# Performance work log

Hardware: AMD Instinct MI355X
Metric: run time of the kernel (lower is better)

## Reference

```python
import jax, jax.numpy as jnp
import numpy as np

N = 100000      # num_nodes
R = 8           # num_relations
D = 128         # hidden_dim
E = 600000      # num_edges
P = 100000      # num query pairs
PH = 128        # pair_hidden_dim


def _xavier(key, shape):
    fan_in, fan_out = shape[-2], shape[-1]
    limit = float(np.sqrt(6.0 / (fan_in + fan_out)))
    return jax.random.uniform(key, shape, jnp.float32, -limit, limit)


def setup_inputs() -> dict:
    key = jax.random.key(0)
    ks = jax.random.split(key, 16)
    edge_index = jax.random.randint(ks[0], (2, E), 0, N)
    edge_type = jax.random.randint(ks[1], (E,), 0, R)
    drug_index = jax.random.randint(ks[2], (P,), 0, N)
    disease_index = jax.random.randint(ks[3], (P,), 0, N)
    emb = _xavier(ks[4], (N, D))
    rw1 = _xavier(ks[5], (R, D, D))
    sl1 = _xavier(ks[6], (D, D))
    b1 = jnp.zeros((D,), jnp.float32)
    rw2 = _xavier(ks[7], (R, D, D))
    sl2 = _xavier(ks[8], (D, D))
    b2 = jnp.zeros((D,), jnp.float32)
    pw1 = _xavier(ks[9], (3 * D, PH))
    pb1 = jnp.zeros((PH,), jnp.float32)
    pw2 = _xavier(ks[10], (PH, 1))
    pb2 = jnp.zeros((1,), jnp.float32)
    return {
        "edge_index": edge_index, "edge_type": edge_type,
        "drug_index": drug_index, "disease_index": disease_index,
        "emb": emb, "rw1": rw1, "sl1": sl1, "b1": b1,
        "rw2": rw2, "sl2": sl2, "b2": b2,
        "pw1": pw1, "pb1": pb1, "pw2": pw2, "pb2": pb2,
    }


def _rgcn_layer(x, rel_w, self_w, bias, src, dst, etype):
    # Transform all node features once per relation: [R, N, D]
    xW = jnp.einsum('nd,rde->rne', x, rel_w)
    # Per-relation in-degree of dst (matches torch bincount-per-relation, clamp_min(1))
    seg_key = etype * N + dst                                  # [E]
    deg = jax.ops.segment_sum(jnp.ones((src.shape[0],), x.dtype), seg_key,
                              num_segments=R * N)
    deg = jnp.maximum(deg, 1.0)
    msg = xW[etype, src] / deg[seg_key][:, None]               # [E, D]
    agg = jax.ops.segment_sum(msg, dst, num_segments=N)        # [N, D]
    return x @ self_w + agg + bias


def reference(edge_index, edge_type, drug_index, disease_index,
              emb, rw1, sl1, b1, rw2, sl2, b2, pw1, pb1, pw2, pb2):
    src, dst = edge_index[0], edge_index[1]
    # encode (eval mode: dropout is identity)
    x = _rgcn_layer(emb, rw1, sl1, b1, src, dst, edge_type)
    x = jax.nn.relu(x)
    x = _rgcn_layer(x, rw2, sl2, b2, src, dst, edge_type)
    # score_pairs
    dh = x[drug_index]
    sh = x[disease_index]
    feat = jnp.concatenate((dh, sh, dh * sh), axis=-1)         # [P, 3D]
    h = jax.nn.relu(feat @ pw1 + pb1)
    logits = (h @ pw2 + pb2)[:, 0]                             # [P]
    return logits
```

## Files before the change

kernel.cpp:

```cpp
#include <hip/hip_runtime.h>

#define D 128
#define RMAX 16

typedef short s16x8 __attribute__((ext_vector_type(8)));
typedef float f32x4 __attribute__((ext_vector_type(4)));

__device__ inline unsigned short f2b(float f) {
    unsigned u = __builtin_bit_cast(unsigned, f);
    unsigned r = (u + 0x7FFFu + ((u >> 16) & 1u)) >> 16;
    return (unsigned short)r;
}
__device__ inline float b2f(unsigned short h) {
    unsigned u = ((unsigned)h) << 16;
    return __builtin_bit_cast(float, u);
}


__global__ void k_count2(const int* __restrict__ etype, const int* __restrict__ dstA,
                         int E, int N, int R,
                         int* __restrict__ deg, int* __restrict__ counts) {
    __shared__ int lh[RMAX];
    if (threadIdx.x < RMAX) lh[threadIdx.x] = 0;
    __syncthreads();
    int e = blockIdx.x * blockDim.x + threadIdx.x;
    if (e < E) {
        int r = etype[e];
        atomicAdd(&deg[r * N + dstA[e]], 1);
        atomicAdd(&lh[r], 1);
    }
    __syncthreads();
    if (threadIdx.x < R && lh[threadIdx.x])
        atomicAdd(&counts[threadIdx.x], lh[threadIdx.x]);
}

__global__ void k_offsets(const int* __restrict__ counts, int* __restrict__ po,
                          int R, int N) {
    if (threadIdx.x == 0 && blockIdx.x == 0) {
        int acc = 0;
        for (int r = 0; r < R; ++r) {
            po[r] = acc;
            acc += ((counts[r] + 127) / 128) * 128;
        }
        po[R] = acc;
        acc += ((N + 127) / 128) * 128;
        po[R + 1] = acc;
    }
}


template<int VPT>
__global__ void k_scan_blk(const int* __restrict__ in, int* __restrict__ tmp,
                           int* __restrict__ bsum, int n) {
    __shared__ int sd[256];
    int t = threadIdx.x;
    long base = (long)blockIdx.x * (256 * VPT) + (long)t * VPT;
    int s[VPT];
    int tsum = 0;
    #pragma unroll
    for (int k = 0; k < VPT; ++k) { s[k] = (base + k < n) ? in[base + k] : 0; tsum += s[k]; }
    sd[t] = tsum;
    __syncthreads();
    for (int off = 1; off < 256; off <<= 1) {
        int v = (t >= off) ? sd[t - off] : 0;
        __syncthreads();
        sd[t] += v;
        __syncthreads();
    }
    int run = sd[t] - tsum;
    #pragma unroll
    for (int k = 0; k < VPT; ++k) { if (base + k < n) tmp[base + k] = run; run += s[k]; }
    if (t == 255) bsum[blockIdx.x] = sd[255];
}

__global__ void k_scan2(const int* __restrict__ bsum, int* __restrict__ boff, int nb) {
    __shared__ int sd[256];
    int t = threadIdx.x;
    int v = (t < nb) ? bsum[t] : 0;
    sd[t] = v;
    __syncthreads();
    for (int off = 1; off < 256; off <<= 1) {
        int w = (t >= off) ? sd[t - off] : 0;
        __syncthreads();
        sd[t] += w;
        __syncthreads();
    }
    if (t < nb) boff[t] = sd[t] - v;
}

__global__ void k_scan3(const int* __restrict__ tmp, const int* __restrict__ boff,
                        int* __restrict__ out, int n, int shift) {
    int i = blockIdx.x * 256 + threadIdx.x;
    if (i < n) out[i] = tmp[i] + boff[i >> shift];
}


__global__ void k_scatter3(const int* __restrict__ etype, const int* __restrict__ srcA,
                           const int* __restrict__ dstA, int E, int N, int R,
                           const int* __restrict__ degOff, const int* __restrict__ po,
                           int* __restrict__ binCur, int* __restrict__ slotSrc) {
    int t = blockIdx.x * 256 + threadIdx.x;
    if (t < E) {
        int r = etype[t];
        int bin = r * N + dstA[t];
        int rank = atomicAdd(&binCur[bin], 1);
        int pos = po[r] + (degOff[bin] - degOff[r * N]) + rank;
        slotSrc[pos] = srcA[t];
    } else if (t < E + N) {
        int n = t - E;
        slotSrc[po[R] + n] = n;
    }
}


__global__ void k_prep(const float* __restrict__ emb,
                       const float* __restrict__ rw1, const float* __restrict__ sl1,
                       const float* __restrict__ rw2, const float* __restrict__ sl2,
                       const float* __restrict__ pw1,
                       unsigned short* __restrict__ embb,
                       unsigned short* __restrict__ wAll1,
                       unsigned short* __restrict__ wAll2,
                       unsigned short* __restrict__ pw1T,
                       int N, int R)
{
    long t = (long)blockIdx.x * 256 + threadIdx.x;
    long u0 = (long)N * D / 4;
    if (t < u0) {
        long i = t * 4;
        f32x4 v = *(const f32x4*)(emb + i);
        unsigned a0 = (unsigned)f2b(v[0]) | ((unsigned)f2b(v[1]) << 16);
        unsigned a1 = (unsigned)f2b(v[2]) | ((unsigned)f2b(v[3]) << 16);
        uint2 o; o.x = a0; o.y = a1;
        *(uint2*)(embb + i) = o;
        return;
    }
    t -= u0;
    long uW = (long)(R + 1) * D * D;
    if (t < 2 * uW) {
        const float* rw = (t < uW) ? rw1 : rw2;
        const float* sl = (t < uW) ? sl1 : sl2;
        unsigned short* o = (t < uW) ? wAll1 : wAll2;
        long u = (t < uW) ? t : t - uW;
        int r = (int)(u >> 14);
        int nb = (int)(u & 16383);
        int n = nb >> 7, kk = nb & 127;
        int ke = kk ^ ((n & 7) << 3);
        float v = (r < R) ? rw[((size_t)r * D + ke) * D + n] : sl[(size_t)ke * D + n];
        o[u] = f2b(v);
        return;
    }
    t -= 2 * uW;
    if (t < 3 * D * D) {
        int n = (int)(t / 384), ck = (int)(t - n * 384);
        int ch = ck >> 7, kl = (ck & 127) ^ ((n & 7) << 3);
        pw1T[t] = f2b(pw1[(size_t)(ch * 128 + kl) * 128 + n]);
    }
}


__global__ __launch_bounds__(256) void k_gemm_msg(
    const unsigned short* __restrict__ xb,
    const unsigned short* __restrict__ wAll,
    const int* __restrict__ slotSrc,
    const int* __restrict__ po, int R,
    unsigned short* __restrict__ y)
{
    __shared__ unsigned char smB[32768];
    int tid = threadIdx.x;
    int row0 = blockIdx.x * 128;
    if (row0 >= po[R + 1]) return;
    int r = 0;
    while (row0 >= po[r + 1]) ++r;

    int lane = tid & 63, wid = tid >> 6;
    int lo = lane & 15, hi = lane >> 4;

    int r0g = wid * 32 + lo, r1g = r0g + 16;
    int sv0 = slotSrc[row0 + r0g];
    int sv1 = slotSrc[row0 + r1g];
    const unsigned short* xrow0 = xb + (size_t)sv0 * D;
    const unsigned short* xrow1 = xb + (size_t)sv1 * D;
    s16x8 a0[4], a1[4];
    #pragma unroll
    for (int ks = 0; ks < 4; ++ks) {
        a0[ks] = *(const s16x8*)(xrow0 + ks * 32 + hi * 8);
        a1[ks] = *(const s16x8*)(xrow1 + ks * 32 + hi * 8);
    }

    {
        const int4* src = (const int4*)(wAll + (size_t)r * D * D);
        int4* dstl = (int4*)smB;
        #pragma unroll
        for (int i = 0; i < 8; ++i) dstl[tid + i * 256] = src[tid + i * 256];
    }
    __syncthreads();

    f32x4 acc[2][8];
    #pragma unroll
    for (int a = 0; a < 2; ++a)
        #pragma unroll
        for (int b = 0; b < 8; ++b) acc[a][b] = (f32x4){0, 0, 0, 0};

    #pragma unroll
    for (int ks = 0; ks < 4; ++ks) {
        int kb = ks * 64 + hi * 16;
        #pragma unroll
        for (int n = 0; n < 8; ++n) {
            int cr = n * 16 + lo;
            s16x8 bf = *(const s16x8*)(smB + cr * 256 + (kb ^ ((cr & 7) << 4)));
            acc[0][n] = __builtin_amdgcn_mfma_f32_16x16x32_bf16(a0[ks], bf, acc[0][n], 0, 0, 0);
            acc[1][n] = __builtin_amdgcn_mfma_f32_16x16x32_bf16(a1[ks], bf, acc[1][n], 0, 0, 0);
        }
    }

    __syncthreads();
    #pragma unroll
    for (int m2 = 0; m2 < 2; ++m2) {
        int rbase = wid * 32 + m2 * 16 + hi * 4;
        #pragma unroll
        for (int reg = 0; reg < 4; ++reg) {
            int rl = rbase + reg;
            #pragma unroll
            for (int n = 0; n < 8; ++n) {
                int byteoff = rl * 256 + (((n * 32 + (lo >> 3) * 16) ^ ((rl & 7) << 4)) + (lo & 7) * 2);
                *(unsigned short*)(smB + byteoff) = f2b(acc[m2][n][reg]);
            }
        }
    }
    __syncthreads();
    {
        int m = tid >> 1, half = tid & 1;
        unsigned short* dst = y + (size_t)(row0 + m) * D;
        #pragma unroll
        for (int i = 0; i < 8; ++i) {
            int c = half * 8 + i;
            int4 v = *(const int4*)(smB + m * 256 + ((c * 16) ^ ((m & 7) << 4)));
            *(int4*)(dst + c * 8) = v;
        }
    }
}


template<bool RELU>
__global__ void k_reduce2(const unsigned short* __restrict__ y,
                          const int* __restrict__ deg, const int* __restrict__ degOff,
                          const int* __restrict__ po,
                          const float* __restrict__ bias,
                          unsigned short* __restrict__ out, int N, int R)
{
    __shared__ int rbase[RMAX + 1];
    int tid = threadIdx.x;
    if (tid <= R) rbase[tid] = (tid < R) ? (po[tid] - degOff[(size_t)tid * N]) : po[R];
    __syncthreads();

    int team = tid >> 4, cj = tid & 15;
    float b[8];
    *(f32x4*)(b)     = *(const f32x4*)(bias + cj * 8);
    *(f32x4*)(b + 4) = *(const f32x4*)(bias + cj * 8 + 4);
    int dbase = blockIdx.x * 64 + team * 4;
    for (int i = 0; i < 4; ++i) {
        int d = dbase + i;
        if (d >= N) return;
        float a[8];
        {
            int4 v = *(const int4*)(y + (size_t)(rbase[R] + d) * D + cj * 8);
            const unsigned short* hp = (const unsigned short*)&v;
            #pragma unroll
            for (int j = 0; j < 8; ++j) a[j] = b[j] + b2f(hp[j]);
        }
        for (int r = 0; r < R; ++r) {
            int bin = r * N + d;
            int len = deg[bin];
            if (!len) continue;
            long start = rbase[r] + degOff[bin];
            float s8[8];
            #pragma unroll
            for (int j = 0; j < 8; ++j) s8[j] = 0.0f;
            for (int q = 0; q < len; ++q) {
                int4 v = *(const int4*)(y + (size_t)(start + q) * D + cj * 8);
                const unsigned short* hp = (const unsigned short*)&v;
                #pragma unroll
                for (int j = 0; j < 8; ++j) s8[j] += b2f(hp[j]);
            }
            float inv = 1.0f / (float)len;
            #pragma unroll
            for (int j = 0; j < 8; ++j) a[j] = fmaf(s8[j], inv, a[j]);
        }
        unsigned short o[8];
        #pragma unroll
        for (int j = 0; j < 8; ++j) {
            float v = RELU ? fmaxf(a[j], 0.0f) : a[j];
            o[j] = f2b(v);
        }
        *(int4*)(out + (size_t)d * D + cj * 8) = *(const int4*)o;
    }
}


__global__ __launch_bounds__(256) void k_score(
    const unsigned short* __restrict__ x2b,
    const int* __restrict__ drug, const int* __restrict__ dis,
    const unsigned short* __restrict__ pw1T,
    const float* __restrict__ pb1, const float* __restrict__ pw2,
    const float* __restrict__ pb2, float* __restrict__ outp, int P)
{
    __shared__ unsigned char smA[32768];
    __shared__ unsigned char smB[32768];
    __shared__ float pb1s[128];
    __shared__ float pw2s[128];
    int tid = threadIdx.x;
    long p0 = (long)blockIdx.x * 128;
    if (tid < 128) { pb1s[tid] = pb1[tid]; pw2s[tid] = pw2[tid]; }
    float pb2v = pb2[0];

    int lane = tid & 63, wid = tid >> 6;
    int lo = lane & 15, hi = lane >> 4;
    f32x4 acc[2][8];
    #pragma unroll
    for (int a = 0; a < 2; ++a)
        #pragma unroll
        for (int b = 0; b < 8; ++b) acc[a][b] = (f32x4){0, 0, 0, 0};

    for (int ch = 0; ch < 3; ++ch) {
        {
            const int4* src = (const int4*)pw1T;
            int4* dstl = (int4*)smB;
            #pragma unroll
            for (int i = 0; i < 8; ++i) {
                int q = tid + i * 256;
                int n = q >> 4, c = q & 15;
                dstl[q] = src[n * 48 + ch * 16 + c];
            }
        }
        {
            int m = tid >> 1, half = tid & 1;
            long p = p0 + m;
            int4 z = {0, 0, 0, 0};
            if (p < P) {
                const int4* da = (const int4*)(x2b + (size_t)drug[p] * D);
                const int4* db = (const int4*)(x2b + (size_t)dis[p] * D);
                for (int c = half * 8; c < half * 8 + 8; ++c) {
                    int4 v;
                    if (ch == 0) v = da[c];
                    else if (ch == 1) v = db[c];
                    else {
                        int4 va = da[c], vb = db[c];
                        const unsigned short* ap = (const unsigned short*)&va;
                        const unsigned short* bp = (const unsigned short*)&vb;
                        unsigned short o[8];
                        #pragma unroll
                        for (int j = 0; j < 8; ++j) o[j] = f2b(b2f(ap[j]) * b2f(bp[j]));
                        v = *(const int4*)o;
                    }
                    *(int4*)(smA + m * 256 + ((c * 16) ^ ((m & 7) << 4))) = v;
                }
            } else {
                for (int c = half * 8; c < half * 8 + 8; ++c)
                    *(int4*)(smA + m * 256 + ((c * 16) ^ ((m & 7) << 4))) = z;
            }
        }
        __syncthreads();

        #pragma unroll
        for (int ks = 0; ks < 4; ++ks) {
            int kb = ks * 64 + hi * 16;
            int r0 = wid * 32 + lo, r1 = r0 + 16;
            s16x8 a0 = *(const s16x8*)(smA + r0 * 256 + (kb ^ ((r0 & 7) << 4)));
            s16x8 a1 = *(const s16x8*)(smA + r1 * 256 + (kb ^ ((r1 & 7) << 4)));
            #pragma unroll
            for (int n = 0; n < 8; ++n) {
                int cr = n * 16 + lo;
                s16x8 bf = *(const s16x8*)(smB + cr * 256 + (kb ^ ((cr & 7) << 4)));
                acc[0][n] = __builtin_amdgcn_mfma_f32_16x16x32_bf16(a0, bf, acc[0][n], 0, 0, 0);
                acc[1][n] = __builtin_amdgcn_mfma_f32_16x16x32_bf16(a1, bf, acc[1][n], 0, 0, 0);
            }
        }
        __syncthreads();
    }

    #pragma unroll
    for (int m2 = 0; m2 < 2; ++m2)
        #pragma unroll
        for (int reg = 0; reg < 4; ++reg) {
            float s = 0.0f;
            #pragma unroll
            for (int n = 0; n < 8; ++n) {
                int col = n * 16 + lo;
                float v = acc[m2][n][reg] + pb1s[col];
                v = fmaxf(v, 0.0f);
                s = fmaf(v, pw2s[col], s);
            }
            s += __shfl_xor(s, 1, 64);
            s += __shfl_xor(s, 2, 64);
            s += __shfl_xor(s, 4, 64);
            s += __shfl_xor(s, 8, 64);
            long p = p0 + wid * 32 + m2 * 16 + hi * 4 + reg;
            if (lo == 0 && p < P) outp[p] = s + pb2v;
        }
}


extern "C" void kernel_launch(void* const* d_in, const int* in_sizes, int n_in,
                              void* d_out, int out_size, void* d_ws, size_t ws_size,
                              hipStream_t stream) {
    const int*   edge_index = (const int*)d_in[0];
    const int*   edge_type  = (const int*)d_in[1];
    const int*   drug       = (const int*)d_in[2];
    const int*   dis        = (const int*)d_in[3];
    const float* emb        = (const float*)d_in[4];
    const float* rw1        = (const float*)d_in[5];
    const float* sl1        = (const float*)d_in[6];
    const float* b1         = (const float*)d_in[7];
    const float* rw2        = (const float*)d_in[8];
    const float* sl2        = (const float*)d_in[9];
    const float* b2         = (const float*)d_in[10];
    const float* pw1        = (const float*)d_in[11];
    const float* pb1        = (const float*)d_in[12];
    const float* pw2        = (const float*)d_in[13];
    const float* pb2        = (const float*)d_in[14];

    const int E = in_sizes[1];
    const int P = in_sizes[2];
    const int N = in_sizes[4] / D;
    const int R = in_sizes[5] / (D * D);

    const int* srcA = edge_index;
    const int* dstA = edge_index + E;

    const int slotN = E + N + 128 * (R + 1);

    char* ws = (char*)d_ws;
    unsigned short* embb = (unsigned short*)ws; ws += (size_t)N * D * 2;
    unsigned short* x1b  = (unsigned short*)ws; ws += (size_t)N * D * 2;
    unsigned short* y    = (unsigned short*)ws; ws += (size_t)slotN * D * 2;
    unsigned short* wAll1 = (unsigned short*)ws; ws += (size_t)(R + 1) * D * D * 2;
    unsigned short* wAll2 = (unsigned short*)ws; ws += (size_t)(R + 1) * D * D * 2;
    unsigned short* pw1T  = (unsigned short*)ws; ws += (size_t)3 * D * D * 2;
    int*   deg     = (int*)ws;   ws += (size_t)R * N * 4;
    int*   binCur  = (int*)ws;   ws += (size_t)R * N * 4;
    int*   counts  = (int*)ws;   ws += 256;
    int*   slotSrc = (int*)ws;   ws += (size_t)slotN * 4;
    size_t zbytes = (size_t)(2 * R * N + 64 + slotN) * 4;
    int* degOff  = (int*)ws; ws += (size_t)R * N * 4;
    int* bsum    = (int*)ws; ws += 256 * 4;
    int* boff    = (int*)ws; ws += 256 * 4;
    int* po      = (int*)ws; ws += 256;
    unsigned short* x2b = embb;

    hipMemsetAsync(deg, 0, zbytes, stream);

    long u0 = (long)N * D / 4;
    long uW = (long)(R + 1) * D * D;
    long utot = u0 + 2 * uW + 3 * D * D;
    k_prep<<<(int)((utot + 255) / 256), 256, 0, stream>>>(emb, rw1, sl1, rw2, sl2, pw1,
                                                          embb, wAll1, wAll2, pw1T, N, R);

    k_count2<<<(E + 255) / 256, 256, 0, stream>>>(edge_type, dstA, E, N, R, deg, counts);
    k_offsets<<<1, 1, 0, stream>>>(counts, po, R, N);

    int nbS = (R * N + 4095) / 4096;
    k_scan_blk<16><<<nbS, 256, 0, stream>>>(deg, degOff, bsum, R * N);
    k_scan2<<<1, 256, 0, stream>>>(bsum, boff, nbS);
    k_scan3<<<(R * N + 255) / 256, 256, 0, stream>>>(degOff, boff, degOff, R * N, 12);

    k_scatter3<<<(E + N + 255) / 256, 256, 0, stream>>>(edge_type, srcA, dstA, E, N, R,
                                                        degOff, po, binCur, slotSrc);

    int gridM = (E + 127) / 128 + (N + 127) / 128 + R + 2;
    int gridR = (N + 63) / 64;

    k_gemm_msg<<<gridM, 256, 0, stream>>>(embb, wAll1, slotSrc, po, R, y);
    k_reduce2<true><<<gridR, 256, 0, stream>>>(y, deg, degOff, po, b1, x1b, N, R);
    k_gemm_msg<<<gridM, 256, 0, stream>>>(x1b, wAll2, slotSrc, po, R, y);
    k_reduce2<false><<<gridR, 256, 0, stream>>>(y, deg, degOff, po, b2, x2b, N, R);
    k_score<<<(P + 127) / 128, 256, 0, stream>>>(x2b, drug, dis, pw1T, pb1, pw2, pb2,
                                                 (float*)d_out, P);
}
```

Before: 508.3 us.

## Split RGCN message GEMM and reduction into two destination-node halves

Destination nodes are split into two halves, and for each layer the message GEMM and the segmented reduction run once per half. Each pass writes a smaller intermediate message buffer, so the reduction can read it back while it is more likely still in cache. Per-relation offsets are now derived from the scanned degree offsets instead of a separate atomic counts histogram, and segment lengths come from adjacent offsets instead of the deg array. The cost is four more kernel launches and a GEMM grid sized for all edges, so many blocks in each half exit early.

```diff
diff --git a/kernel.cpp b/kernel.cpp
--- a/kernel.cpp
+++ b/kernel.cpp
@@ -18,34 +18,9 @@
 
 
 __global__ void k_count2(const int* __restrict__ etype, const int* __restrict__ dstA,
-                         int E, int N, int R,
-                         int* __restrict__ deg, int* __restrict__ counts) {
-    __shared__ int lh[RMAX];
-    if (threadIdx.x < RMAX) lh[threadIdx.x] = 0;
-    __syncthreads();
+                         int E, int N, int* __restrict__ deg) {
     int e = blockIdx.x * blockDim.x + threadIdx.x;
-    if (e < E) {
-        int r = etype[e];
-        atomicAdd(&deg[r * N + dstA[e]], 1);
-        atomicAdd(&lh[r], 1);
-    }
-    __syncthreads();
-    if (threadIdx.x < R && lh[threadIdx.x])
-        atomicAdd(&counts[threadIdx.x], lh[threadIdx.x]);
-}
-
-__global__ void k_offsets(const int* __restrict__ counts, int* __restrict__ po,
-                          int R, int N) {
-    if (threadIdx.x == 0 && blockIdx.x == 0) {
-        int acc = 0;
-        for (int r = 0; r < R; ++r) {
-            po[r] = acc;
-            acc += ((counts[r] + 127) / 128) * 128;
-        }
-        po[R] = acc;
-        acc += ((N + 127) / 128) * 128;
-        po[R + 1] = acc;
-    }
+    if (e < E) atomicAdd(&deg[etype[e] * N + dstA[e]], 1);
 }
 
 
@@ -95,20 +70,48 @@
 }
 
 
+__global__ void k_offsets(const int* __restrict__ degOff, int* __restrict__ po,
+                          int R, int N, int Nh, int E) {
+    if (threadIdx.x == 0 && blockIdx.x == 0) {
+        int acc = 0;
+        for (int h = 0; h < 2; ++h) {
+            int d0 = h ? Nh : 0;
+            int d1 = h ? N : Nh;
+            for (int r = 0; r < R; ++r) {
+                int o0 = degOff[(size_t)r * N + d0];
+                int o1;
+                if (d1 == N) o1 = (r == R - 1) ? E : degOff[(size_t)(r + 1) * N];
+                else         o1 = degOff[(size_t)r * N + d1];
+                int c = o1 - o0;
+                po[h * (R + 1) + r] = acc;
+                acc += ((c + 127) / 128) * 128;
+            }
+            po[h * (R + 1) + R] = acc;
+            acc += (((d1 - d0) + 127) / 128) * 128;
+        }
+        po[2 * (R + 1)] = acc;
+    }
+}
+
+
 __global__ void k_scatter3(const int* __restrict__ etype, const int* __restrict__ srcA,
-                           const int* __restrict__ dstA, int E, int N, int R,
+                           const int* __restrict__ dstA, int E, int N, int R, int Nh,
                            const int* __restrict__ degOff, const int* __restrict__ po,
                            int* __restrict__ binCur, int* __restrict__ slotSrc) {
     int t = blockIdx.x * 256 + threadIdx.x;
     if (t < E) {
         int r = etype[t];
-        int bin = r * N + dstA[t];
+        int d = dstA[t];
+        int h = (d >= Nh) ? 1 : 0;
+        int bin = r * N + d;
         int rank = atomicAdd(&binCur[bin], 1);
-        int pos = po[r] + (degOff[bin] - degOff[r * N]) + rank;
+        int base = degOff[(size_t)r * N + (h ? Nh : 0)];
+        int pos = po[h * (R + 1) + r] + (degOff[bin] - base) + rank;
         slotSrc[pos] = srcA[t];
     } else if (t < E + N) {
         int n = t - E;
-        slotSrc[po[R] + n] = n;
+        int h = (n >= Nh) ? 1 : 0;
+        slotSrc[po[h * (R + 1) + R] + (n - (h ? Nh : 0))] = n;
     }
 }
 
@@ -162,15 +165,16 @@
     const unsigned short* __restrict__ xb,
     const unsigned short* __restrict__ wAll,
     const int* __restrict__ slotSrc,
-    const int* __restrict__ po, int R,
+    const int* __restrict__ po, int R, int h,
     unsigned short* __restrict__ y)
 {
     __shared__ unsigned char smB[32768];
     int tid = threadIdx.x;
-    int row0 = blockIdx.x * 128;
-    if (row0 >= po[R + 1]) return;
-    int r = 0;
-    while (row0 >= po[r + 1]) ++r;
+    int row0 = po[h * (R + 1)] + blockIdx.x * 128;
+    if (row0 >= po[(h + 1) * (R + 1)]) return;
+    int s = h * (R + 1);
+    while (row0 >= po[s + 1]) ++s;
+    int rw = s - h * (R + 1);
 
     int lane = tid & 63, wid = tid >> 6;
     int lo = lane & 15, hi = lane >> 4;
@@ -188,7 +192,7 @@
     }
 
     {
-        const int4* src = (const int4*)(wAll + (size_t)r * D * D);
+        const int4* src = (const int4*)(wAll + (size_t)rw * D * D);
         int4* dstl = (int4*)smB;
         #pragma unroll
         for (int i = 0; i < 8; ++i) dstl[tid + i * 256] = src[tid + i * 256];
@@ -243,24 +247,28 @@
 
 template<bool RELU>
 __global__ void k_reduce2(const unsigned short* __restrict__ y,
-                          const int* __restrict__ deg, const int* __restrict__ degOff,
-                          const int* __restrict__ po,
+                          const int* __restrict__ degOff, const int* __restrict__ po,
                           const float* __restrict__ bias,
-                          unsigned short* __restrict__ out, int N, int R)
+                          unsigned short* __restrict__ out,
+                          int N, int R, int E, int h, int d0, int dcnt)
 {
     __shared__ int rbase[RMAX + 1];
     int tid = threadIdx.x;
-    if (tid <= R) rbase[tid] = (tid < R) ? (po[tid] - degOff[(size_t)tid * N]) : po[R];
+    if (tid <= R) {
+        if (tid < R) rbase[tid] = po[h * (R + 1) + tid] - degOff[(size_t)tid * N + d0];
+        else         rbase[R]   = po[h * (R + 1) + R] - d0;
+    }
     __syncthreads();
 
     int team = tid >> 4, cj = tid & 15;
     float b[8];
     *(f32x4*)(b)     = *(const f32x4*)(bias + cj * 8);
     *(f32x4*)(b + 4) = *(const f32x4*)(bias + cj * 8 + 4);
-    int dbase = blockIdx.x * 64 + team * 4;
+    int dbase = d0 + blockIdx.x * 64 + team * 4;
+    int dend = d0 + dcnt;
     for (int i = 0; i < 4; ++i) {
         int d = dbase + i;
-        if (d >= N) return;
+        if (d >= dend) return;
         float a[8];
         {
             int4 v = *(const int4*)(y + (size_t)(rbase[R] + d) * D + cj * 8);
@@ -270,9 +278,11 @@
         }
         for (int r = 0; r < R; ++r) {
             int bin = r * N + d;
-            int len = deg[bin];
+            int o0 = degOff[bin];
+            int o1 = (bin + 1 < R * N) ? degOff[bin + 1] : E;
+            int len = o1 - o0;
             if (!len) continue;
-            long start = rbase[r] + degOff[bin];
+            long start = rbase[r] + o0;
             float s8[8];
             #pragma unroll
             for (int j = 0; j < 8; ++j) s8[j] = 0.0f;
@@ -423,11 +433,12 @@
     const int P = in_sizes[2];
     const int N = in_sizes[4] / D;
     const int R = in_sizes[5] / (D * D);
+    const int Nh = (N + 1) / 2;
 
     const int* srcA = edge_index;
     const int* dstA = edge_index + E;
 
-    const int slotN = E + N + 128 * (R + 1);
+    const int slotN = E + N + 128 * (2 * R + 4);
 
     char* ws = (char*)d_ws;
     unsigned short* embb = (unsigned short*)ws; ws += (size_t)N * D * 2;
@@ -438,9 +449,8 @@
     unsigned short* pw1T  = (unsigned short*)ws; ws += (size_t)3 * D * D * 2;
     int*   deg     = (int*)ws;   ws += (size_t)R * N * 4;
     int*   binCur  = (int*)ws;   ws += (size_t)R * N * 4;
-    int*   counts  = (int*)ws;   ws += 256;
     int*   slotSrc = (int*)ws;   ws += (size_t)slotN * 4;
-    size_t zbytes = (size_t)(2 * R * N + 64 + slotN) * 4;
+    size_t zbytes = (size_t)(2 * R * N + slotN) * 4;
     int* degOff  = (int*)ws; ws += (size_t)R * N * 4;
     int* bsum    = (int*)ws; ws += 256 * 4;
     int* boff    = (int*)ws; ws += 256 * 4;
@@ -455,24 +465,30 @@
     k_prep<<<(int)((utot + 255) / 256), 256, 0, stream>>>(emb, rw1, sl1, rw2, sl2, pw1,
                                                           embb, wAll1, wAll2, pw1T, N, R);
 
-    k_count2<<<(E + 255) / 256, 256, 0, stream>>>(edge_type, dstA, E, N, R, deg, counts);
-    k_offsets<<<1, 1, 0, stream>>>(counts, po, R, N);
+    k_count2<<<(E + 255) / 256, 256, 0, stream>>>(edge_type, dstA, E, N, deg);
 
     int nbS = (R * N + 4095) / 4096;
     k_scan_blk<16><<<nbS, 256, 0, stream>>>(deg, degOff, bsum, R * N);
     k_scan2<<<1, 256, 0, stream>>>(bsum, boff, nbS);
     k_scan3<<<(R * N + 255) / 256, 256, 0, stream>>>(degOff, boff, degOff, R * N, 12);
 
+    k_offsets<<<1, 1, 0, stream>>>(degOff, po, R, N, Nh, E);
+
     k_scatter3<<<(E + N + 255) / 256, 256, 0, stream>>>(edge_type, srcA, dstA, E, N, R,
-                                                        degOff, po, binCur, slotSrc);
-
-    int gridM = (E + 127) / 128 + (N + 127) / 128 + R + 2;
-    int gridR = (N + 63) / 64;
-
-    k_gemm_msg<<<gridM, 256, 0, stream>>>(embb, wAll1, slotSrc, po, R, y);
-    k_reduce2<true><<<gridR, 256, 0, stream>>>(y, deg, degOff, po, b1, x1b, N, R);
-    k_gemm_msg<<<gridM, 256, 0, stream>>>(x1b, wAll2, slotSrc, po, R, y);
-    k_reduce2<false><<<gridR, 256, 0, stream>>>(y, deg, degOff, po, b2, x2b, N, R);
+                                                        Nh, degOff, po, binCur, slotSrc);
+
+    int gridMh = (E + 127) / 128 + (Nh + 127) / 128 + R + 2;
+    int gridR0 = (Nh + 63) / 64;
+    int gridR1 = (N - Nh + 63) / 64;
+
+    k_gemm_msg<<<gridMh, 256, 0, stream>>>(embb, wAll1, slotSrc, po, R, 0, y);
+    k_reduce2<true><<<gridR0, 256, 0, stream>>>(y, degOff, po, b1, x1b, N, R, E, 0, 0, Nh);
+    k_gemm_msg<<<gridMh, 256, 0, stream>>>(embb, wAll1, slotSrc, po, R, 1, y);
+    k_reduce2<true><<<gridR1, 256, 0, stream>>>(y, degOff, po, b1, x1b, N, R, E, 1, Nh, N - Nh);
+    k_gemm_msg<<<gridMh, 256, 0, stream>>>(x1b, wAll2, slotSrc, po, R, 0, y);
+    k_reduce2<false><<<gridR0, 256, 0, stream>>>(y, degOff, po, b2, x2b, N, R, E, 0, 0, Nh);
+    k_gemm_msg<<<gridMh, 256, 0, stream>>>(x1b, wAll2, slotSrc, po, R, 1, y);
+    k_reduce2<false><<<gridR1, 256, 0, stream>>>(y, degOff, po, b2, x2b, N, R, E, 1, Nh, N - Nh);
     k_score<<<(P + 127) / 128, 256, 0, stream>>>(x2b, drug, dis, pw1T, pb1, pw2, pb2,
                                                  (float*)d_out, P);
 }
```

Result: slower. 565.2 us (+11.2%).

## Fuse per-relation message GEMM with degree-normalized reduction per destination tile

Applied to the files above, without the earlier changes.

Replaces the separate message GEMM plus reduce kernels with one fused kernel per layer. Each block owns 128 destination nodes and loops over relations, running the gathered GEMM on that relation's edge slice and accumulating normalized results from shared memory into per-thread fp32 registers. This removes the large intermediate y buffer round trip, the padded per-relation offsets, and the count/offset kernels. In exchange it has only about 782 blocks, a serial per-thread slot loop over 128-row chunks, 64 float accumulators per thread that can lower occupancy, and a weight reload per relation per block.

```diff
diff --git a/kernel.cpp b/kernel.cpp
--- a/kernel.cpp
+++ b/kernel.cpp
@@ -1,7 +1,6 @@
 #include <hip/hip_runtime.h>
 
 #define D 128
-#define RMAX 16
 
 typedef short s16x8 __attribute__((ext_vector_type(8)));
 typedef float f32x4 __attribute__((ext_vector_type(4)));
@@ -18,34 +17,9 @@
 
 
 __global__ void k_count2(const int* __restrict__ etype, const int* __restrict__ dstA,
-                         int E, int N, int R,
-                         int* __restrict__ deg, int* __restrict__ counts) {
-    __shared__ int lh[RMAX];
-    if (threadIdx.x < RMAX) lh[threadIdx.x] = 0;
-    __syncthreads();
+                         int E, int N, int* __restrict__ deg) {
     int e = blockIdx.x * blockDim.x + threadIdx.x;
-    if (e < E) {
-        int r = etype[e];
-        atomicAdd(&deg[r * N + dstA[e]], 1);
-        atomicAdd(&lh[r], 1);
-    }
-    __syncthreads();
-    if (threadIdx.x < R && lh[threadIdx.x])
-        atomicAdd(&counts[threadIdx.x], lh[threadIdx.x]);
-}
-
-__global__ void k_offsets(const int* __restrict__ counts, int* __restrict__ po,
-                          int R, int N) {
-    if (threadIdx.x == 0 && blockIdx.x == 0) {
-        int acc = 0;
-        for (int r = 0; r < R; ++r) {
-            po[r] = acc;
-            acc += ((counts[r] + 127) / 128) * 128;
-        }
-        po[R] = acc;
-        acc += ((N + 127) / 128) * 128;
-        po[R + 1] = acc;
-    }
+    if (e < E) atomicAdd(&deg[etype[e] * N + dstA[e]], 1);
 }
 
 
@@ -95,20 +69,15 @@
 }
 
 
-__global__ void k_scatter3(const int* __restrict__ etype, const int* __restrict__ srcA,
-                           const int* __restrict__ dstA, int E, int N, int R,
-                           const int* __restrict__ degOff, const int* __restrict__ po,
-                           int* __restrict__ binCur, int* __restrict__ slotSrc) {
-    int t = blockIdx.x * 256 + threadIdx.x;
-    if (t < E) {
-        int r = etype[t];
-        int bin = r * N + dstA[t];
+__global__ void k_scatter(const int* __restrict__ etype, const int* __restrict__ srcA,
+                          const int* __restrict__ dstA, int E, int N,
+                          const int* __restrict__ degOff, int* __restrict__ binCur,
+                          int* __restrict__ slotSrc) {
+    int e = blockIdx.x * 256 + threadIdx.x;
+    if (e < E) {
+        int bin = etype[e] * N + dstA[e];
         int rank = atomicAdd(&binCur[bin], 1);
-        int pos = po[r] + (degOff[bin] - degOff[r * N]) + rank;
-        slotSrc[pos] = srcA[t];
-    } else if (t < E + N) {
-        int n = t - E;
-        slotSrc[po[R] + n] = n;
+        slotSrc[degOff[bin] + rank] = srcA[e];
     }
 }
 
@@ -158,141 +127,144 @@
 }
 
 
-__global__ __launch_bounds__(256) void k_gemm_msg(
+template<bool RELU>
+__global__ __launch_bounds__(256) void k_fused(
     const unsigned short* __restrict__ xb,
     const unsigned short* __restrict__ wAll,
     const int* __restrict__ slotSrc,
-    const int* __restrict__ po, int R,
-    unsigned short* __restrict__ y)
+    const int* __restrict__ degOff,
+    const float* __restrict__ bias,
+    unsigned short* __restrict__ out,
+    int N, int R, int E)
 {
     __shared__ unsigned char smB[32768];
+    __shared__ unsigned char smM[32768];
     int tid = threadIdx.x;
-    int row0 = blockIdx.x * 128;
-    if (row0 >= po[R + 1]) return;
-    int r = 0;
-    while (row0 >= po[r + 1]) ++r;
+    int d0 = blockIdx.x * 128;
+    int dmax = (d0 + 128 < N) ? d0 + 128 : N;
 
     int lane = tid & 63, wid = tid >> 6;
     int lo = lane & 15, hi = lane >> 4;
-
-    int r0g = wid * 32 + lo, r1g = r0g + 16;
-    int sv0 = slotSrc[row0 + r0g];
-    int sv1 = slotSrc[row0 + r1g];
-    const unsigned short* xrow0 = xb + (size_t)sv0 * D;
-    const unsigned short* xrow1 = xb + (size_t)sv1 * D;
-    s16x8 a0[4], a1[4];
+    int m = tid >> 1, ch = tid & 1;
+    int dmine = d0 + m;
+
+    float a[64];
     #pragma unroll
-    for (int ks = 0; ks < 4; ++ks) {
-        a0[ks] = *(const s16x8*)(xrow0 + ks * 32 + hi * 8);
-        a1[ks] = *(const s16x8*)(xrow1 + ks * 32 + hi * 8);
-    }
-
-    {
-        const int4* src = (const int4*)(wAll + (size_t)r * D * D);
-        int4* dstl = (int4*)smB;
+    for (int j = 0; j < 64; ++j) a[j] = 0.0f;
+
+    for (int r = 0; r <= R; ++r) {
+        int s0, cnt;
+        if (r < R) {
+            s0 = degOff[r * N + d0];
+            int b1 = r * N + dmax;
+            int s1 = (b1 < R * N) ? degOff[b1] : E;
+            cnt = s1 - s0;
+            if (cnt == 0) continue;
+        } else {
+            s0 = 0;
+            cnt = dmax - d0;
+        }
+
+        {
+            const int4* src = (const int4*)(wAll + (size_t)r * D * D);
+            int4* dstl = (int4*)smB;
+            #pragma unroll
+            for (int i = 0; i < 8; ++i) dstl[tid + i * 256] = src[tid + i * 256];
+        }
+        __syncthreads();
+
+        for (int c0 = 0; c0 < cnt; c0 += 128) {
+            int i0 = c0 + wid * 32 + lo;
+            int i1 = i0 + 16;
+            int ci0 = (i0 < cnt) ? i0 : cnt - 1;
+            int ci1 = (i1 < cnt) ? i1 : cnt - 1;
+            int sv0, sv1;
+            if (r < R) { sv0 = slotSrc[s0 + ci0]; sv1 = slotSrc[s0 + ci1]; }
+            else       { sv0 = d0 + ci0;          sv1 = d0 + ci1; }
+            const unsigned short* xr0 = xb + (size_t)sv0 * D;
+            const unsigned short* xr1 = xb + (size_t)sv1 * D;
+            s16x8 af0[4], af1[4];
+            #pragma unroll
+            for (int ks = 0; ks < 4; ++ks) {
+                af0[ks] = *(const s16x8*)(xr0 + ks * 32 + hi * 8);
+                af1[ks] = *(const s16x8*)(xr1 + ks * 32 + hi * 8);
+            }
+
+            f32x4 acc[2][8];
+            #pragma unroll
+            for (int q = 0; q < 2; ++q)
+                #pragma unroll
+                for (int n = 0; n < 8; ++n) acc[q][n] = (f32x4){0, 0, 0, 0};
+
+            #pragma unroll
+            for (int ks = 0; ks < 4; ++ks) {
+                int kb = ks * 64 + hi * 16;
+                #pragma unroll
+                for (int n = 0; n < 8; ++n) {
+                    int cr = n * 16 + lo;
+                    s16x8 bf = *(const s16x8*)(smB + cr * 256 + (kb ^ ((cr & 7) << 4)));
+                    acc[0][n] = __builtin_amdgcn_mfma_f32_16x16x32_bf16(af0[ks], bf, acc[0][n], 0, 0, 0);
+                    acc[1][n] = __builtin_amdgcn_mfma_f32_16x16x32_bf16(af1[ks], bf, acc[1][n], 0, 0, 0);
+                }
+            }
+
+            __syncthreads();
+            #pragma unroll
+            for (int m2 = 0; m2 < 2; ++m2) {
+                int rbase = wid * 32 + m2 * 16 + hi * 4;
+                #pragma unroll
+                for (int reg = 0; reg < 4; ++reg) {
+                    int rl = rbase + reg;
+                    #pragma unroll
+                    for (int n = 0; n < 8; ++n) {
+                        int byteoff = rl * 256 + (((n * 32 + (lo >> 3) * 16) ^ ((rl & 7) << 4)) + (lo & 7) * 2);
+                        *(unsigned short*)(smM + byteoff) = f2b(acc[m2][n][reg]);
+                    }
+                }
+            }
+            __syncthreads();
+
+            if (dmine < N) {
+                int st, en; float inv;
+                if (r < R) {
+                    int bin = r * N + dmine;
+                    st = degOff[bin];
+                    en = (bin + 1 < R * N) ? degOff[bin + 1] : E;
+                    inv = (en > st) ? 1.0f / (float)(en - st) : 0.0f;
+                } else {
+                    st = m; en = m + 1; inv = 1.0f;
+                }
+                int loI = st > s0 + c0 ? st : s0 + c0;
+                int hiI = en < s0 + c0 + 128 ? en : s0 + c0 + 128;
+                for (int slot = loI; slot < hiI; ++slot) {
+                    int rl = slot - (s0 + c0);
+                    #pragma unroll
+                    for (int g = 0; g < 8; ++g) {
+                        int c = ch * 8 + g;
+                        int4 v = *(const int4*)(smM + rl * 256 + ((c * 16) ^ ((rl & 7) << 4)));
+                        const unsigned short* hp = (const unsigned short*)&v;
+                        #pragma unroll
+                        for (int k = 0; k < 8; ++k)
+                            a[g * 8 + k] = fmaf(b2f(hp[k]), inv, a[g * 8 + k]);
+                    }
+                }
+            }
+            __syncthreads();
+        }
+    }
+
+    if (dmine < N) {
         #pragma unroll
-        for (int i = 0; i < 8; ++i) dstl[tid + i * 256] = src[tid + i * 256];
-    }
-    __syncthreads();
-
-    f32x4 acc[2][8];
-    #pragma unroll
-    for (int a = 0; a < 2; ++a)
-        #pragma unroll
-        for (int b = 0; b < 8; ++b) acc[a][b] = (f32x4){0, 0, 0, 0};
-
-    #pragma unroll
-    for (int ks = 0; ks < 4; ++ks) {
-        int kb = ks * 64 + hi * 16;
-        #pragma unroll
-        for (int n = 0; n < 8; ++n) {
-            int cr = n * 16 + lo;
-            s16x8 bf = *(const s16x8*)(smB + cr * 256 + (kb ^ ((cr & 7) << 4)));
-            acc[0][n] = __builtin_amdgcn_mfma_f32_16x16x32_bf16(a0[ks], bf, acc[0][n], 0, 0, 0);
-            acc[1][n] = __builtin_amdgcn_mfma_f32_16x16x32_bf16(a1[ks], bf, acc[1][n], 0, 0, 0);
-        }
-    }
-
-    __syncthreads();
-    #pragma unroll
-    for (int m2 = 0; m2 < 2; ++m2) {
-        int rbase = wid * 32 + m2 * 16 + hi * 4;
-        #pragma unroll
-        for (int reg = 0; reg < 4; ++reg) {
-            int rl = rbase + reg;
-            #pragma unroll
-            for (int n = 0; n < 8; ++n) {
-                int byteoff = rl * 256 + (((n * 32 + (lo >> 3) * 16) ^ ((rl & 7) << 4)) + (lo & 7) * 2);
-                *(unsigned short*)(smB + byteoff) = f2b(acc[m2][n][reg]);
-            }
-        }
-    }
-    __syncthreads();
-    {
-        int m = tid >> 1, half = tid & 1;
-        unsigned short* dst = y + (size_t)(row0 + m) * D;
-        #pragma unroll
-        for (int i = 0; i < 8; ++i) {
-            int c = half * 8 + i;
-            int4 v = *(const int4*)(smB + m * 256 + ((c * 16) ^ ((m & 7) << 4)));
-            *(int4*)(dst + c * 8) = v;
-        }
-    }
-}
-
-
-template<bool RELU>
-__global__ void k_reduce2(const unsigned short* __restrict__ y,
-                          const int* __restrict__ deg, const int* __restrict__ degOff,
-                          const int* __restrict__ po,
-                          const float* __restrict__ bias,
-                          unsigned short* __restrict__ out, int N, int R)
-{
-    __shared__ int rbase[RMAX + 1];
-    int tid = threadIdx.x;
-    if (tid <= R) rbase[tid] = (tid < R) ? (po[tid] - degOff[(size_t)tid * N]) : po[R];
-    __syncthreads();
-
-    int team = tid >> 4, cj = tid & 15;
-    float b[8];
-    *(f32x4*)(b)     = *(const f32x4*)(bias + cj * 8);
-    *(f32x4*)(b + 4) = *(const f32x4*)(bias + cj * 8 + 4);
-    int dbase = blockIdx.x * 64 + team * 4;
-    for (int i = 0; i < 4; ++i) {
-        int d = dbase + i;
-        if (d >= N) return;
-        float a[8];
-        {
-            int4 v = *(const int4*)(y + (size_t)(rbase[R] + d) * D + cj * 8);
-            const unsigned short* hp = (const unsigned short*)&v;
-            #pragma unroll
-            for (int j = 0; j < 8; ++j) a[j] = b[j] + b2f(hp[j]);
-        }
-        for (int r = 0; r < R; ++r) {
-            int bin = r * N + d;
-            int len = deg[bin];
-            if (!len) continue;
-            long start = rbase[r] + degOff[bin];
-            float s8[8];
-            #pragma unroll
-            for (int j = 0; j < 8; ++j) s8[j] = 0.0f;
-            for (int q = 0; q < len; ++q) {
-                int4 v = *(const int4*)(y + (size_t)(start + q) * D + cj * 8);
-                const unsigned short* hp = (const unsigned short*)&v;
-                #pragma unroll
-                for (int j = 0; j < 8; ++j) s8[j] += b2f(hp[j]);
-            }
-            float inv = 1.0f / (float)len;
-            #pragma unroll
-            for (int j = 0; j < 8; ++j) a[j] = fmaf(s8[j], inv, a[j]);
-        }
-        unsigned short o[8];
-        #pragma unroll
-        for (int j = 0; j < 8; ++j) {
-            float v = RELU ? fmaxf(a[j], 0.0f) : a[j];
-            o[j] = f2b(v);
-        }
-        *(int4*)(out + (size_t)d * D + cj * 8) = *(const int4*)o;
+        for (int g = 0; g < 8; ++g) {
+            unsigned short o8[8];
+            #pragma unroll
+            for (int k = 0; k < 8; ++k) {
+                float v = a[g * 8 + k] + bias[ch * 64 + g * 8 + k];
+                if (RELU) v = fmaxf(v, 0.0f);
+                o8[k] = f2b(v);
+            }
+            *(int4*)(out + (size_t)dmine * D + ch * 64 + g * 8) = *(const int4*)o8;
+        }
     }
 }
 
@@ -317,11 +289,11 @@
     int lo = lane & 15, hi = lane >> 4;
     f32x4 acc[2][8];
     #pragma unroll
-    for (int a = 0; a < 2; ++a)
+    for (int q = 0; q < 2; ++q)
         #pragma unroll
-        for (int b = 0; b < 8; ++b) acc[a][b] = (f32x4){0, 0, 0, 0};
-
-    for (int ch = 0; ch < 3; ++ch) {
+        for (int b = 0; b < 8; ++b) acc[q][b] = (f32x4){0, 0, 0, 0};
+
+    for (int chn = 0; chn < 3; ++chn) {
         {
             const int4* src = (const int4*)pw1T;
             int4* dstl = (int4*)smB;
@@ -329,7 +301,7 @@
             for (int i = 0; i < 8; ++i) {
                 int q = tid + i * 256;
                 int n = q >> 4, c = q & 15;
-                dstl[q] = src[n * 48 + ch * 16 + c];
+                dstl[q] = src[n * 48 + chn * 16 + c];
             }
         }
         {
@@ -341,8 +313,8 @@
                 const int4* db = (const int4*)(x2b + (size_t)dis[p] * D);
                 for (int c = half * 8; c < half * 8 + 8; ++c) {
                     int4 v;
-                    if (ch == 0) v = da[c];
-                    else if (ch == 1) v = db[c];
+                    if (chn == 0) v = da[c];
+                    else if (chn == 1) v = db[c];
                     else {
                         int4 va = da[c], vb = db[c];
                         const unsigned short* ap = (const unsigned short*)&va;
@@ -427,24 +399,19 @@
     const int* srcA = edge_index;
     const int* dstA = edge_index + E;
 
-    const int slotN = E + N + 128 * (R + 1);
-
     char* ws = (char*)d_ws;
     unsigned short* embb = (unsigned short*)ws; ws += (size_t)N * D * 2;
     unsigned short* x1b  = (unsigned short*)ws; ws += (size_t)N * D * 2;
-    unsigned short* y    = (unsigned short*)ws; ws += (size_t)slotN * D * 2;
     unsigned short* wAll1 = (unsigned short*)ws; ws += (size_t)(R + 1) * D * D * 2;
     unsigned short* wAll2 = (unsigned short*)ws; ws += (size_t)(R + 1) * D * D * 2;
     unsigned short* pw1T  = (unsigned short*)ws; ws += (size_t)3 * D * D * 2;
-    int*   deg     = (int*)ws;   ws += (size_t)R * N * 4;
-    int*   binCur  = (int*)ws;   ws += (size_t)R * N * 4;
-    int*   counts  = (int*)ws;   ws += 256;
-    int*   slotSrc = (int*)ws;   ws += (size_t)slotN * 4;
-    size_t zbytes = (size_t)(2 * R * N + 64 + slotN) * 4;
+    int* deg     = (int*)ws; ws += (size_t)R * N * 4;
+    int* binCur  = (int*)ws; ws += (size_t)R * N * 4;
+    size_t zbytes = (size_t)(2 * R * N) * 4;
+    int* slotSrc = (int*)ws; ws += (size_t)E * 4;
     int* degOff  = (int*)ws; ws += (size_t)R * N * 4;
     int* bsum    = (int*)ws; ws += 256 * 4;
     int* boff    = (int*)ws; ws += 256 * 4;
-    int* po      = (int*)ws; ws += 256;
     unsigned short* x2b = embb;
 
     hipMemsetAsync(deg, 0, zbytes, stream);
@@ -455,24 +422,21 @@
     k_prep<<<(int)((utot + 255) / 256), 256, 0, stream>>>(emb, rw1, sl1, rw2, sl2, pw1,
                                                           embb, wAll1, wAll2, pw1T, N, R);
 
-    k_count2<<<(E + 255) / 256, 256, 0, stream>>>(edge_type, dstA, E, N, R, deg, counts);
-    k_offsets<<<1, 1, 0, stream>>>(counts, po, R, N);
+    k_count2<<<(E + 255) / 256, 256, 0, stream>>>(edge_type, dstA, E, N, deg);
 
     int nbS = (R * N + 4095) / 4096;
     k_scan_blk<16><<<nbS, 256, 0, stream>>>(deg, degOff, bsum, R * N);
     k_scan2<<<1, 256, 0, stream>>>(bsum, boff, nbS);
     k_scan3<<<(R * N + 255) / 256, 256, 0, stream>>>(degOff, boff, degOff, R * N, 12);
 
-    k_scatter3<<<(E + N + 255) / 256, 256, 0, stream>>>(edge_type, srcA, dstA, E, N, R,
-                                                        degOff, po, binCur, slotSrc);
-
-    int gridM = (E + 127) / 128 + (N + 127) / 128 + R + 2;
-    int gridR = (N + 63) / 64;
-
-    k_gemm_msg<<<gridM, 256, 0, stream>>>(embb, wAll1, slotSrc, po, R, y);
-    k_reduce2<true><<<gridR, 256, 0, stream>>>(y, deg, degOff, po, b1, x1b, N, R);
-    k_gemm_msg<<<gridM, 256, 0, stream>>>(x1b, wAll2, slotSrc, po, R, y);
-    k_reduce2<false><<<gridR, 256, 0, stream>>>(y, deg, degOff, po, b2, x2b, N, R);
+    k_scatter<<<(E + 255) / 256, 256, 0, stream>>>(edge_type, srcA, dstA, E, N,
+                                                   degOff, binCur, slotSrc);
+
+    int gridF = (N + 127) / 128;
+
+    k_fused<true><<<gridF, 256, 0, stream>>>(embb, wAll1, slotSrc, degOff, b1, x1b, N, R, E);
+    k_fused<false><<<gridF, 256, 0, stream>>>(x1b, wAll2, slotSrc, degOff, b2, x2b, N, R, E);
+
     k_score<<<(P + 127) / 128, 256, 0, stream>>>(x2b, drug, dis, pw1T, pb1, pw2, pb2,
                                                  (float*)d_out, P);
 }
```

New measurement: 520.6 us. 2.4% more time.

## Read GEMM weights directly from global and use per-wave output staging

Applied to the files above, without the earlier changes.

The message GEMM no longer copies the 32KB relation weight tile into shared memory. Each wave reads its B fragments straight from global or L2, using an unswizzled weight layout. The output is staged in a per-wave LDS region, which removes the block-wide barriers, and launch bounds now request 4 blocks per SM. The reduce kernel derives bin lengths from adjacent degOff entries instead of reading a separate deg array. The risk is redundant global weight loads per wave and a degOff-based length that may be wrong across relation boundaries.

```diff
diff --git a/kernel.cpp b/kernel.cpp
--- a/kernel.cpp
+++ b/kernel.cpp
@@ -144,8 +144,7 @@
         int r = (int)(u >> 14);
         int nb = (int)(u & 16383);
         int n = nb >> 7, kk = nb & 127;
-        int ke = kk ^ ((n & 7) << 3);
-        float v = (r < R) ? rw[((size_t)r * D + ke) * D + n] : sl[(size_t)ke * D + n];
+        float v = (r < R) ? rw[((size_t)r * D + kk) * D + n] : sl[(size_t)kk * D + n];
         o[u] = f2b(v);
         return;
     }
@@ -158,14 +157,14 @@
 }
 
 
-__global__ __launch_bounds__(256) void k_gemm_msg(
+__global__ __launch_bounds__(256, 4) void k_gemm_msg(
     const unsigned short* __restrict__ xb,
     const unsigned short* __restrict__ wAll,
     const int* __restrict__ slotSrc,
     const int* __restrict__ po, int R,
     unsigned short* __restrict__ y)
 {
-    __shared__ unsigned char smB[32768];
+    __shared__ unsigned char stg[32768];
     int tid = threadIdx.x;
     int row0 = blockIdx.x * 128;
     if (row0 >= po[R + 1]) return;
@@ -187,54 +186,43 @@
         a1[ks] = *(const s16x8*)(xrow1 + ks * 32 + hi * 8);
     }
 
-    {
-        const int4* src = (const int4*)(wAll + (size_t)r * D * D);
-        int4* dstl = (int4*)smB;
-        #pragma unroll
-        for (int i = 0; i < 8; ++i) dstl[tid + i * 256] = src[tid + i * 256];
-    }
-    __syncthreads();
-
     f32x4 acc[2][8];
     #pragma unroll
-    for (int a = 0; a < 2; ++a)
-        #pragma unroll
-        for (int b = 0; b < 8; ++b) acc[a][b] = (f32x4){0, 0, 0, 0};
-
+    for (int q = 0; q < 2; ++q)
+        #pragma unroll
+        for (int n = 0; n < 8; ++n) acc[q][n] = (f32x4){0, 0, 0, 0};
+
+    const unsigned short* Bp = wAll + (size_t)r * D * D;
     #pragma unroll
     for (int ks = 0; ks < 4; ++ks) {
-        int kb = ks * 64 + hi * 16;
         #pragma unroll
         for (int n = 0; n < 8; ++n) {
-            int cr = n * 16 + lo;
-            s16x8 bf = *(const s16x8*)(smB + cr * 256 + (kb ^ ((cr & 7) << 4)));
+            s16x8 bf = *(const s16x8*)(Bp + (size_t)(n * 16 + lo) * D + ks * 32 + hi * 8);
             acc[0][n] = __builtin_amdgcn_mfma_f32_16x16x32_bf16(a0[ks], bf, acc[0][n], 0, 0, 0);
             acc[1][n] = __builtin_amdgcn_mfma_f32_16x16x32_bf16(a1[ks], bf, acc[1][n], 0, 0, 0);
         }
     }
 
-    __syncthreads();
+    unsigned char* wreg = stg + wid * 8192;
     #pragma unroll
     for (int m2 = 0; m2 < 2; ++m2) {
-        int rbase = wid * 32 + m2 * 16 + hi * 4;
         #pragma unroll
         for (int reg = 0; reg < 4; ++reg) {
-            int rl = rbase + reg;
+            int rloc = m2 * 16 + hi * 4 + reg;
             #pragma unroll
             for (int n = 0; n < 8; ++n) {
-                int byteoff = rl * 256 + (((n * 32 + (lo >> 3) * 16) ^ ((rl & 7) << 4)) + (lo & 7) * 2);
-                *(unsigned short*)(smB + byteoff) = f2b(acc[m2][n][reg]);
-            }
-        }
-    }
-    __syncthreads();
+                int byteoff = rloc * 256 + (((n * 32 + (lo >> 3) * 16) ^ ((rloc & 7) << 4)) + (lo & 7) * 2);
+                *(unsigned short*)(wreg + byteoff) = f2b(acc[m2][n][reg]);
+            }
+        }
+    }
     {
-        int m = tid >> 1, half = tid & 1;
-        unsigned short* dst = y + (size_t)(row0 + m) * D;
+        int m = lane >> 1, half = lane & 1;
+        unsigned short* dst = y + (size_t)(row0 + wid * 32 + m) * D;
         #pragma unroll
         for (int i = 0; i < 8; ++i) {
             int c = half * 8 + i;
-            int4 v = *(const int4*)(smB + m * 256 + ((c * 16) ^ ((m & 7) << 4)));
+            int4 v = *(const int4*)(wreg + m * 256 + ((c * 16) ^ ((m & 7) << 4)));
             *(int4*)(dst + c * 8) = v;
         }
     }
@@ -243,10 +231,10 @@
 
 template<bool RELU>
 __global__ void k_reduce2(const unsigned short* __restrict__ y,
-                          const int* __restrict__ deg, const int* __restrict__ degOff,
+                          const int* __restrict__ degOff,
                           const int* __restrict__ po,
                           const float* __restrict__ bias,
-                          unsigned short* __restrict__ out, int N, int R)
+                          unsigned short* __restrict__ out, int N, int R, int E)
 {
     __shared__ int rbase[RMAX + 1];
     int tid = threadIdx.x;
@@ -270,9 +258,11 @@
         }
         for (int r = 0; r < R; ++r) {
             int bin = r * N + d;
-            int len = deg[bin];
+            int o0 = degOff[bin];
+            int o1 = (bin + 1 < R * N) ? degOff[bin + 1] : E;
+            int len = o1 - o0;
             if (!len) continue;
-            long start = rbase[r] + degOff[bin];
+            long start = rbase[r] + o0;
             float s8[8];
             #pragma unroll
             for (int j = 0; j < 8; ++j) s8[j] = 0.0f;
@@ -317,11 +307,11 @@
     int lo = lane & 15, hi = lane >> 4;
     f32x4 acc[2][8];
     #pragma unroll
-    for (int a = 0; a < 2; ++a)
-        #pragma unroll
-        for (int b = 0; b < 8; ++b) acc[a][b] = (f32x4){0, 0, 0, 0};
-
-    for (int ch = 0; ch < 3; ++ch) {
+    for (int q = 0; q < 2; ++q)
+        #pragma unroll
+        for (int b = 0; b < 8; ++b) acc[q][b] = (f32x4){0, 0, 0, 0};
+
+    for (int chn = 0; chn < 3; ++chn) {
         {
             const int4* src = (const int4*)pw1T;
             int4* dstl = (int4*)smB;
@@ -329,7 +319,7 @@
             for (int i = 0; i < 8; ++i) {
                 int q = tid + i * 256;
                 int n = q >> 4, c = q & 15;
-                dstl[q] = src[n * 48 + ch * 16 + c];
+                dstl[q] = src[n * 48 + chn * 16 + c];
             }
         }
         {
@@ -341,8 +331,8 @@
                 const int4* db = (const int4*)(x2b + (size_t)dis[p] * D);
                 for (int c = half * 8; c < half * 8 + 8; ++c) {
                     int4 v;
-                    if (ch == 0) v = da[c];
-                    else if (ch == 1) v = db[c];
+                    if (chn == 0) v = da[c];
+                    else if (chn == 1) v = db[c];
                     else {
                         int4 va = da[c], vb = db[c];
                         const unsigned short* ap = (const unsigned short*)&va;
@@ -427,7 +417,7 @@
     const int* srcA = edge_index;
     const int* dstA = edge_index + E;
 
-    const int slotN = E + N + 128 * (R + 1);
+    const int slotN = E + N + 128 * (R + 2);
 
     char* ws = (char*)d_ws;
     unsigned short* embb = (unsigned short*)ws; ws += (size_t)N * D * 2;
@@ -470,9 +460,9 @@
     int gridR = (N + 63) / 64;
 
     k_gemm_msg<<<gridM, 256, 0, stream>>>(embb, wAll1, slotSrc, po, R, y);
-    k_reduce2<true><<<gridR, 256, 0, stream>>>(y, deg, degOff, po, b1, x1b, N, R);
+    k_reduce2<true><<<gridR, 256, 0, stream>>>(y, degOff, po, b1, x1b, N, R, E);
     k_gemm_msg<<<gridM, 256, 0, stream>>>(x1b, wAll2, slotSrc, po, R, y);
-    k_reduce2<false><<<gridR, 256, 0, stream>>>(y, deg, degOff, po, b2, x2b, N, R);
+    k_reduce2<false><<<gridR, 256, 0, stream>>>(y, degOff, po, b2, x2b, N, R, E);
     k_score<<<(P + 127) / 128, 256, 0, stream>>>(x2b, drug, dis, pw1T, pb1, pw2, pb2,
                                                  (float*)d_out, P);
 }
```

Result: slower. 561.1 us (+10.4%).
